# Kernel optimization log

Measured on AMD Instinct MI355X. Metric: run time of the kernel, lower is better.

Reference implementation:

```python
import jax, jax.numpy as jnp
import numpy as np

HIDDEN = 1024
HEADS = 16
HEAD_DIM = HIDDEN // HEADS
B, T = 4, 2048


def setup_inputs() -> dict:
    key = jax.random.key(0)
    k_x, k_w1, k_b1, k_w2, k_b2 = jax.random.split(key, 5)
    lim1 = 1.0 / np.sqrt(HIDDEN)
    x = jax.random.normal(k_x, (B, T, HIDDEN), dtype=jnp.float32)
    # causal lower-triangular mask, broadcastable to [B, H, T, T]
    mask = jnp.tril(jnp.ones((T, T), dtype=jnp.int32))[None, None, :, :]
    # qkv_proj: Linear(HIDDEN, 3*HIDDEN); torch Linear: y = x @ W.T + b
    W_qkv = jax.random.uniform(k_w1, (3 * HIDDEN, HIDDEN), minval=-lim1, maxval=lim1, dtype=jnp.float32)
    b_qkv = jax.random.uniform(k_b1, (3 * HIDDEN,), minval=-lim1, maxval=lim1, dtype=jnp.float32)
    W_out = jax.random.uniform(k_w2, (HIDDEN, HIDDEN), minval=-lim1, maxval=lim1, dtype=jnp.float32)
    b_out = jax.random.uniform(k_b2, (HIDDEN,), minval=-lim1, maxval=lim1, dtype=jnp.float32)
    return {"x": x, "mask": mask, "W_qkv": W_qkv, "b_qkv": b_qkv, "W_out": W_out, "b_out": b_out}


def reference(x, mask, W_qkv, b_qkv, W_out, b_out):
    Bx, Tx, C = x.shape
    qkv = x @ W_qkv.T + b_qkv                      # [B, T, 3C]
    qkv = qkv.reshape(Bx, Tx, 3, HEADS, HEAD_DIM)
    qkv = jnp.transpose(qkv, (2, 0, 3, 1, 4))      # [3, B, H, T, Dh]
    Q, K, V = qkv[0], qkv[1], qkv[2]
    scale = 1.0 / np.sqrt(HEAD_DIM)
    scores = jnp.einsum('bhqd,bhkd->bhqk', Q, K) * scale  # [B, H, T, T]
    scores = jnp.where(mask == 0, -jnp.inf, scores)
    probs = jax.nn.softmax(scores, axis=-1)
    ctx = jnp.einsum('bhqk,bhkd->bhqd', probs, V)  # [B, H, T, Dh]
    ctx = jnp.transpose(ctx, (0, 2, 1, 3)).reshape(Bx, Tx, C)
    return ctx @ W_out.T + b_out
```

## Files before the change

### kernel.cpp

```cpp
#include <hip/hip_runtime.h>
#include <cstdint>
#include <cstddef>

#define B_ 4
#define T_ 2048
#define C_ 1024
#define H_ 16
#define D_ 64

typedef __attribute__((ext_vector_type(8))) __bf16 bf16x8;
typedef __attribute__((ext_vector_type(4))) float floatx4;

#define QSCL (0.125f * 1.44269504088896f)
#define FMAX 24.0f

__device__ __forceinline__ unsigned short f2bf(float f) {
  union { float f; unsigned int u; } v; v.f = f;
  unsigned int r = v.u + 0x7fffu + ((v.u >> 16) & 1u);
  return (unsigned short)(r >> 16);
}
__device__ __forceinline__ ushort4 pk4(float a, float b, float c, float d) {
  ushort4 u; u.x = f2bf(a); u.y = f2bf(b); u.z = f2bf(c); u.w = f2bf(d);
  return u;
}
__device__ __forceinline__ bf16x8 cvt8(float4 a, float4 b) {
  bf16x8 r;
  r[0] = a.x; r[1] = a.y; r[2] = a.z; r[3] = a.w;
  r[4] = b.x; r[5] = b.y; r[6] = b.z; r[7] = b.w;
  return r;
}
__device__ __forceinline__ unsigned pkbf2(float a, float b) {
  union { __bf16 h[2]; unsigned u; } w;
  w.h[0] = (__bf16)a; w.h[1] = (__bf16)b;
  return w.u;
}

__device__ __forceinline__ void gl_lds16(const void* g, void* l) {
  __builtin_amdgcn_global_load_lds(
      (const __attribute__((address_space(1))) unsigned int*)g,
      (__attribute__((address_space(3))) unsigned int*)l, 16, 0, 0);
}

__global__ __launch_bounds__(256)
void conv_bf16(const float* __restrict__ src, unsigned short* __restrict__ dst,
               int n8) {
  for (int i = blockIdx.x * 256 + threadIdx.x; i < n8; i += gridDim.x * 256) {
    const float4* s = (const float4*)src + 2 * (size_t)i;
    float4 a = s[0], b = s[1];
    ((bf16x8*)dst)[i] = cvt8(a, b);
  }
}

__global__ __launch_bounds__(256)
void conv_tri(const float* __restrict__ s1, unsigned short* __restrict__ d1, int n1,
              const float* __restrict__ s2, unsigned short* __restrict__ d2, int n2,
              const float* __restrict__ s3, unsigned short* __restrict__ d3, int n3) {
  for (int i = blockIdx.x * 256 + threadIdx.x; i < n1 + n2 + n3; i += gridDim.x * 256) {
    const float4* sp; bf16x8* dp;
    if (i < n1)           { sp = (const float4*)s1 + 2 * (size_t)i;       dp = (bf16x8*)d1 + i; }
    else if (i < n1 + n2) { int j = i - n1;      sp = (const float4*)s2 + 2 * (size_t)j; dp = (bf16x8*)d2 + j; }
    else                  { int j = i - n1 - n2; sp = (const float4*)s3 + 2 * (size_t)j; dp = (bf16x8*)d3 + j; }
    float4 a = sp[0], b = sp[1];
    *dp = cvt8(a, b);
  }
}

template<int EPI, int GATHER, int WBF>
__global__ __launch_bounds__(256, 2)
void gemm_bt(const unsigned short* __restrict__ Abf,
             const void* __restrict__ Wraw,
             const float* __restrict__ bias,
             float* __restrict__ out,
             unsigned short* __restrict__ qws,
             unsigned short* __restrict__ kws,
             unsigned short* __restrict__ vtws)
{
  alignas(16) __shared__ unsigned short As[2][128 * 64];
  alignas(16) __shared__ unsigned short Bs[2][WBF ? 128 * 64 : 128 * 72];
  const int tid  = threadIdx.x;
  const int lane = tid & 63;
  const int wid  = tid >> 6;
  const int col  = lane & 15;
  const int quad = lane >> 4;
  const int wm = (wid >> 1) << 6;
  const int wn = (wid & 1) << 6;
  const int bm = blockIdx.y << 7;
  const int bn = blockIdx.x << 7;

  const float* Wf          = (const float*)Wraw;
  const unsigned short* Wb = (const unsigned short*)Wraw;

  const int r0 = tid >> 3;
  const int c0 = tid & 7;

  floatx4 acc[4][4];
#pragma unroll
  for (int i = 0; i < 4; ++i)
#pragma unroll
    for (int j = 0; j < 4; ++j)
      acc[i][j] = (floatx4){0.f, 0.f, 0.f, 0.f};

#define GSTAGE(k0_, nb_)                                                      \
  do {                                                                        \
    _Pragma("unroll") for (int s = 0; s < 4; ++s) {                           \
      const int row  = (s << 5) + r0;                             \
      const int colE = ((c0 ^ (row & 7)) << 3);             \
      const unsigned short* gsrc;                                             \
      if (GATHER) {                                                           \
        const int m = bm + row;                                               \
        const int b = m >> 11, t = m & 2047;                                  \
        const int hh = (k0_) >> 6;                        \
        gsrc = Abf + ((((size_t)(b * 16 + hh) << 11) + t) << 6) + colE;       \
      } else {                                                                \
        gsrc = Abf + (size_t)(bm + row) * 1024 + (k0_) + colE;                \
      }                                                                       \
      gl_lds16(gsrc, (char*)&As[nb_][0] + (s << 12) + (wid << 10));           \
      if (WBF) {                                                              \
        const unsigned short* ws2 = Wb + (size_t)(bn + row) * 1024 + (k0_) + colE; \
        gl_lds16(ws2, (char*)&Bs[nb_][0] + (s << 12) + (wid << 10));          \
      } else {                                                                \
        const int kc = c0 << 3;                                               \
        const float* wsrc = &Wf[(size_t)(bn + row) * 1024 + (k0_) + kc];      \
        float4 w0 = *(const float4*)wsrc;                                     \
        float4 w1 = *(const float4*)(wsrc + 4);                               \
        *(bf16x8*)&Bs[nb_][row * 72 + kc] = cvt8(w0, w1);                     \
      }                                                                       \
    }                                                                         \
  } while (0)

  GSTAGE(0, 0);
  __syncthreads();

  for (int kt = 0; kt < 16; ++kt) {
    const int buf = kt & 1;
    if (kt + 1 < 16) GSTAGE((kt + 1) << 6, buf ^ 1);

#pragma unroll
    for (int kk = 0; kk < 64; kk += 32) {
      bf16x8 af[4], bfr[4];
#pragma unroll
      for (int i = 0; i < 4; ++i) {
        const int r = wm + i * 16 + col;
        af[i] = *(const bf16x8*)&As[buf][(r << 6) + ((kk + quad * 8) ^ ((r & 7) << 3))];
      }
#pragma unroll
      for (int j = 0; j < 4; ++j) {
        const int r = wn + j * 16 + col;
        if (WBF)
          bfr[j] = *(const bf16x8*)&Bs[buf][(r << 6) + ((kk + quad * 8) ^ ((r & 7) << 3))];
        else
          bfr[j] = *(const bf16x8*)&Bs[buf][r * 72 + kk + quad * 8];
      }
#pragma unroll
      for (int i = 0; i < 4; ++i)
#pragma unroll
        for (int j = 0; j < 4; ++j)
          acc[i][j] = __builtin_amdgcn_mfma_f32_16x16x32_bf16(af[i], bfr[j], acc[i][j], 0, 0, 0);
    }

    __syncthreads();
  }
#undef GSTAGE

#pragma unroll
  for (int i = 0; i < 4; ++i) {
    const int row = bm + wm + i * 16 + quad * 4;
#pragma unroll
    for (int j = 0; j < 4; ++j) {
      const int n  = bn + wn + j * 16 + col;
      const float bv = bias[n];
      float v[4];
#pragma unroll
      for (int r = 0; r < 4; ++r) v[r] = acc[i][j][r] + bv;

      if (EPI == 1) {
#pragma unroll
        for (int r = 0; r < 4; ++r)
          out[(size_t)(row + r) * 1024 + n] = v[r];
      } else {
        const int s   = n >> 10;
        const int rem = n & 1023;
        const int h   = rem >> 6;
        const int d   = rem & 63;
        const int b   = row >> 11;
        const int t   = row & 2047;
        const size_t bh = (size_t)(b * H_ + h);
        if (s == 0) {
#pragma unroll
          for (int r = 0; r < 4; ++r)
            qws[(bh * T_ + t + r) * D_ + d] = f2bf(v[r] * QSCL);
        } else if (s == 1) {
#pragma unroll
          for (int r = 0; r < 4; ++r)
            kws[(bh * T_ + t + r) * D_ + d] = f2bf(v[r]);
        } else {
          *(ushort4*)&vtws[(bh * D_ + d) * T_ + t] = pk4(v[0], v[1], v[2], v[3]);
        }
      }
    }
  }
}

__global__ __launch_bounds__(256, 2)
void attn_causal(unsigned short* __restrict__ qws,
                 const unsigned short* __restrict__ kws,
                 const unsigned short* __restrict__ vtws)
{
  alignas(16) __shared__ unsigned short Ks[2][64 * 64];
  alignas(16) __shared__ unsigned short Vs[2][64 * 64];
  const int tid  = threadIdx.x;
  const int lane = tid & 63;
  const int wid  = tid >> 6;
  const int col  = lane & 15;
  const int quad = lane >> 4;

  const int bh   = blockIdx.x & 63;
  const int band = 15 - (blockIdx.x >> 6);

  const unsigned short* Kp  = kws + (size_t)bh * T_ * D_;
  const unsigned short* Vtp = vtws + (size_t)bh * D_ * T_;

  bf16x8 vones;
#pragma unroll
  for (int i = 0; i < 8; ++i) vones[i] = (__bf16)1.0f;

  const int srow8 = lane >> 3;
  const int swz   = ((lane & 7) ^ srow8) << 3;

#define STAGE(kt_, b_)                                                        \
  do {                                                                        \
    _Pragma("unroll") for (int c2 = 0; c2 < 2; ++c2) {                        \
      const int cb = wid + (c2 << 2);                   \
      gl_lds16(Kp + ((size_t)(((kt_) << 6) + (cb << 3) + srow8) << 6) + swz,  \
               (char*)&Ks[b_][0] + (cb << 10));                               \
      gl_lds16(Vtp + ((size_t)((cb << 3) + srow8) << 11) + ((kt_) << 6) + swz,\
               (char*)&Vs[b_][0] + (cb << 10));                               \
    }                                                                         \
  } while (0)

  const int nk = (band << 1) + 2;
  const int q0 = (band << 7) + (wid << 5);
  unsigned short* Qp = qws + ((size_t)bh * T_ + q0) * D_;

  bf16x8 bq[2][2];
#pragma unroll
  for (int h = 0; h < 2; ++h) {
    bq[h][0] = *(const bf16x8*)&Qp[(h * 16 + col) * D_ + quad * 8];
    bq[h][1] = *(const bf16x8*)&Qp[(h * 16 + col) * D_ + 32 + quad * 8];
  }

  floatx4 o[2][4], ol[2];
#pragma unroll
  for (int h = 0; h < 2; ++h) {
    ol[h] = (floatx4){0.f, 0.f, 0.f, 0.f};
#pragma unroll
    for (int j = 0; j < 4; ++j) o[h][j] = (floatx4){0.f, 0.f, 0.f, 0.f};
  }

  STAGE(0, 0);
  __syncthreads();

  for (int kt = 0; kt < nk; ++kt) {
    const int buf = kt & 1;
    if (kt + 1 < nk) STAGE(kt + 1, buf ^ 1);

    const unsigned short* Kb = &Ks[buf][0];
    bf16x8 kA[4], kB[4];
#pragma unroll
    for (int g = 0; g < 4; ++g) {
      const int r = g * 16 + col;
      kA[g] = *(const bf16x8*)&Kb[(r << 6) + ((quad ^ (col & 7)) << 3)];
      kB[g] = *(const bf16x8*)&Kb[(r << 6) + (((quad | 4) ^ (col & 7)) << 3)];
    }

    floatx4 s[2][4];
    __builtin_amdgcn_s_setprio(1);
#pragma unroll
    for (int h = 0; h < 2; ++h)
#pragma unroll
      for (int g = 0; g < 4; ++g) {
        s[h][g] = (floatx4){-FMAX, -FMAX, -FMAX, -FMAX};
        s[h][g] = __builtin_amdgcn_mfma_f32_16x16x32_bf16(kA[g], bq[h][0], s[h][g], 0, 0, 0);
        s[h][g] = __builtin_amdgcn_mfma_f32_16x16x32_bf16(kB[g], bq[h][1], s[h][g], 0, 0, 0);
      }
    __builtin_amdgcn_s_setprio(0);

    const unsigned short* Vb = &Vs[buf][0];
    bf16x8 vA[4], vB[4];
#pragma unroll
    for (int j = 0; j < 4; ++j) {
      const int r = j * 16 + col;
      vA[j] = *(const bf16x8*)&Vb[(r << 6) + ((quad ^ (col & 7)) << 3)];
      vB[j] = *(const bf16x8*)&Vb[(r << 6) + (((quad | 4) ^ (col & 7)) << 3)];
    }

    if (kt >= nk - 2) {
#pragma unroll
      for (int h = 0; h < 2; ++h) {
        const int lim = q0 - (kt << 6) + (h << 4) + col;
#pragma unroll
        for (int g = 0; g < 4; ++g)
#pragma unroll
          for (int r = 0; r < 4; ++r)
            if (g * 16 + quad * 4 + r > lim) s[h][g][r] = -1e30f;
      }
    }

#pragma unroll
    for (int h = 0; h < 2; ++h)
#pragma unroll
      for (int g = 0; g < 4; ++g)
#pragma unroll
        for (int r = 0; r < 4; ++r)
          s[h][g][r] = __builtin_amdgcn_exp2f(s[h][g][r]);

    __builtin_amdgcn_s_setprio(1);
#pragma unroll
    for (int h = 0; h < 2; ++h) {
      unsigned dw[4][2];
#pragma unroll
      for (int g = 0; g < 4; ++g) {
        dw[g][0] = pkbf2(s[h][g][0], s[h][g][1]);
        dw[g][1] = pkbf2(s[h][g][2], s[h][g][3]);
      }
      unsigned aw[4], bw[4];
      {
        auto t = __builtin_amdgcn_permlane32_swap(dw[0][0], dw[1][0], false, false);
        auto u = __builtin_amdgcn_permlane16_swap(t[0], t[1], false, false);
        aw[0] = u[0]; aw[2] = u[1];
      }
      {
        auto t = __builtin_amdgcn_permlane32_swap(dw[0][1], dw[1][1], false, false);
        auto u = __builtin_amdgcn_permlane16_swap(t[0], t[1], false, false);
        aw[1] = u[0]; aw[3] = u[1];
      }
      {
        auto t = __builtin_amdgcn_permlane32_swap(dw[2][0], dw[3][0], false, false);
        auto u = __builtin_amdgcn_permlane16_swap(t[0], t[1], false, false);
        bw[0] = u[0]; bw[2] = u[1];
      }
      {
        auto t = __builtin_amdgcn_permlane32_swap(dw[2][1], dw[3][1], false, false);
        auto u = __builtin_amdgcn_permlane16_swap(t[0], t[1], false, false);
        bw[1] = u[0]; bw[3] = u[1];
      }
      union { unsigned u[4]; bf16x8 v; } pa0, pa1;
#pragma unroll
      for (int w = 0; w < 4; ++w) { pa0.u[w] = aw[w]; pa1.u[w] = bw[w]; }

#pragma unroll
      for (int j = 0; j < 4; ++j) {
        o[h][j] = __builtin_amdgcn_mfma_f32_16x16x32_bf16(pa0.v, vA[j], o[h][j], 0, 0, 0);
        o[h][j] = __builtin_amdgcn_mfma_f32_16x16x32_bf16(pa1.v, vB[j], o[h][j], 0, 0, 0);
      }
      ol[h] = __builtin_amdgcn_mfma_f32_16x16x32_bf16(pa0.v, vones, ol[h], 0, 0, 0);
      ol[h] = __builtin_amdgcn_mfma_f32_16x16x32_bf16(pa1.v, vones, ol[h], 0, 0, 0);
    }
    __builtin_amdgcn_s_setprio(0);

    __syncthreads();
  }

#pragma unroll
  for (int h = 0; h < 2; ++h) {
    float lr[4];
#pragma unroll
    for (int r = 0; r < 4; ++r) lr[r] = 1.0f / ol[h][r];
#pragma unroll
    for (int j = 0; j < 4; ++j)
#pragma unroll
      for (int r = 0; r < 4; ++r)
        Qp[(size_t)(h * 16 + quad * 4 + r) * D_ + j * 16 + col] =
            f2bf(o[h][j][r] * lr[r]);
  }
#undef STAGE
}

extern "C" void kernel_launch(void* const* d_in, const int* in_sizes, int n_in,
                              void* d_out, int out_size, void* d_ws, size_t ws_size,
                              hipStream_t stream) {
  const float* x     = (const float*)d_in[0];
  const float* W_qkv = (const float*)d_in[2];
  const float* b_qkv = (const float*)d_in[3];
  const float* W_out = (const float*)d_in[4];
  const float* b_out = (const float*)d_in[5];
  float* out = (float*)d_out;

  const size_t per = (size_t)B_ * H_ * T_ * D_;
  unsigned short* qws  = (unsigned short*)d_ws;
  unsigned short* vtws = qws + per;
  unsigned short* kws  = (unsigned short*)d_out;
  unsigned short* xbf  = kws + per;

  const bool bigws  = ws_size >= (size_t)38 * 1024 * 1024;
  const bool hugews = ws_size >= (size_t)40 * 1024 * 1024;
  unsigned short* wqbf = vtws + per;
  unsigned short* wobf = wqbf + (size_t)3 * C_ * C_;

  if (hugews) {
    conv_tri<<<dim3(2048), 256, 0, stream>>>(
        x, xbf, (int)(per >> 3),
        W_qkv, wqbf, (3 * C_ * C_) >> 3,
        W_out, wobf, (C_ * C_) >> 3);
    gemm_bt<0, 0, 1><<<dim3(3072 / 128, 8192 / 128), 256, 0, stream>>>(
        xbf, (const void*)wqbf, b_qkv, nullptr, qws, kws, vtws);
  } else if (bigws) {
    conv_tri<<<dim3(2048), 256, 0, stream>>>(
        x, xbf, (int)(per >> 3),
        W_qkv, wqbf, (3 * C_ * C_) >> 3,
        nullptr, nullptr, 0);
    gemm_bt<0, 0, 1><<<dim3(3072 / 128, 8192 / 128), 256, 0, stream>>>(
        xbf, (const void*)wqbf, b_qkv, nullptr, qws, kws, vtws);
  } else {
    conv_bf16<<<dim3(2048), 256, 0, stream>>>(x, xbf, (int)(per >> 3));
    gemm_bt<0, 0, 0><<<dim3(3072 / 128, 8192 / 128), 256, 0, stream>>>(
        xbf, (const void*)W_qkv, b_qkv, nullptr, qws, kws, vtws);
  }

  attn_causal<<<dim3(16 * 64), 256, 0, stream>>>(qws, kws, vtws);

  if (hugews) {
    gemm_bt<1, 1, 1><<<dim3(1024 / 128, 8192 / 128), 256, 0, stream>>>(
        qws, (const void*)wobf, b_out, out, nullptr, nullptr, nullptr);
  } else {
    conv_bf16<<<dim3(512), 256, 0, stream>>>(W_out, vtws, (C_ * C_) >> 3);
    gemm_bt<1, 1, 1><<<dim3(1024 / 128, 8192 / 128), 256, 0, stream>>>(
        qws, (const void*)vtws, b_out, out, nullptr, nullptr, nullptr);
  }
}
```

Baseline: 247.3 us.

## Enlarge attention query tile to 256 rows per block with per-wave diagonal skip

Each attention block now covers 256 query rows instead of 128, with each wave handling 64 rows split into four 16-row groups processed in two pairs. K/V tiles staged in LDS are therefore reused by twice as many queries, which halves global K/V traffic. Waves skip key tiles past their own diagonal, and only the diagonal tile is masked. The cost is half as many blocks (512), more registers per wave, and load imbalance because waves within a block finish causal work at different tile counts while still waiting at the barriers.

After: 261.9 us. +5.9%, slower.

```diff
diff --git a/kernel.cpp b/kernel.cpp
--- a/kernel.cpp
+++ b/kernel.cpp
@@ -215,7 +215,7 @@
   const int quad = lane >> 4;
 
   const int bh   = blockIdx.x & 63;
-  const int band = 15 - (blockIdx.x >> 6);
+  const int band = 7 - (blockIdx.x >> 6);
 
   const unsigned short* Kp  = kws + (size_t)bh * T_ * D_;
   const unsigned short* Vtp = vtws + (size_t)bh * D_ * T_;
@@ -238,20 +238,21 @@
     }                                                                         \
   } while (0)
 
-  const int nk = (band << 1) + 2;
-  const int q0 = (band << 7) + (wid << 5);
+  const int nk    = (band + 1) << 2;
+  const int kdiag = (band << 2) + wid;
+  const int q0    = (band << 8) + (wid << 6);
   unsigned short* Qp = qws + ((size_t)bh * T_ + q0) * D_;
 
-  bf16x8 bq[2][2];
-#pragma unroll
-  for (int h = 0; h < 2; ++h) {
+  bf16x8 bq[4][2];
+#pragma unroll
+  for (int h = 0; h < 4; ++h) {
     bq[h][0] = *(const bf16x8*)&Qp[(h * 16 + col) * D_ + quad * 8];
     bq[h][1] = *(const bf16x8*)&Qp[(h * 16 + col) * D_ + 32 + quad * 8];
   }
 
-  floatx4 o[2][4], ol[2];
-#pragma unroll
-  for (int h = 0; h < 2; ++h) {
+  floatx4 o[4][4], ol[4];
+#pragma unroll
+  for (int h = 0; h < 4; ++h) {
     ol[h] = (floatx4){0.f, 0.f, 0.f, 0.f};
 #pragma unroll
     for (int j = 0; j < 4; ++j) o[h][j] = (floatx4){0.f, 0.f, 0.f, 0.f};
@@ -264,105 +265,112 @@
     const int buf = kt & 1;
     if (kt + 1 < nk) STAGE(kt + 1, buf ^ 1);
 
-    const unsigned short* Kb = &Ks[buf][0];
-    bf16x8 kA[4], kB[4];
-#pragma unroll
-    for (int g = 0; g < 4; ++g) {
-      const int r = g * 16 + col;
-      kA[g] = *(const bf16x8*)&Kb[(r << 6) + ((quad ^ (col & 7)) << 3)];
-      kB[g] = *(const bf16x8*)&Kb[(r << 6) + (((quad | 4) ^ (col & 7)) << 3)];
+    if (kt <= kdiag) {
+      const unsigned short* Kb = &Ks[buf][0];
+      bf16x8 kA[4], kB[4];
+#pragma unroll
+      for (int g = 0; g < 4; ++g) {
+        const int r = g * 16 + col;
+        kA[g] = *(const bf16x8*)&Kb[(r << 6) + ((quad ^ (col & 7)) << 3)];
+        kB[g] = *(const bf16x8*)&Kb[(r << 6) + (((quad | 4) ^ (col & 7)) << 3)];
+      }
+      const unsigned short* Vb = &Vs[buf][0];
+      bf16x8 vA[4], vB[4];
+#pragma unroll
+      for (int j = 0; j < 4; ++j) {
+        const int r = j * 16 + col;
+        vA[j] = *(const bf16x8*)&Vb[(r << 6) + ((quad ^ (col & 7)) << 3)];
+        vB[j] = *(const bf16x8*)&Vb[(r << 6) + (((quad | 4) ^ (col & 7)) << 3)];
+      }
+
+#pragma unroll
+      for (int hp = 0; hp < 2; ++hp) {
+        floatx4 s[2][4];
+        __builtin_amdgcn_s_setprio(1);
+#pragma unroll
+        for (int hh = 0; hh < 2; ++hh) {
+          const int h = hp * 2 + hh;
+#pragma unroll
+          for (int g = 0; g < 4; ++g) {
+            s[hh][g] = (floatx4){-FMAX, -FMAX, -FMAX, -FMAX};
+            s[hh][g] = __builtin_amdgcn_mfma_f32_16x16x32_bf16(kA[g], bq[h][0], s[hh][g], 0, 0, 0);
+            s[hh][g] = __builtin_amdgcn_mfma_f32_16x16x32_bf16(kB[g], bq[h][1], s[hh][g], 0, 0, 0);
+          }
+        }
+        __builtin_amdgcn_s_setprio(0);
+
+        if (kt == kdiag) {
+#pragma unroll
+          for (int hh = 0; hh < 2; ++hh) {
+            const int lim = ((hp * 2 + hh) << 4) + col;
+#pragma unroll
+            for (int g = 0; g < 4; ++g)
+#pragma unroll
+              for (int r = 0; r < 4; ++r)
+                if (g * 16 + quad * 4 + r > lim) s[hh][g][r] = -1e30f;
+          }
+        }
+
+#pragma unroll
+        for (int hh = 0; hh < 2; ++hh)
+#pragma unroll
+          for (int g = 0; g < 4; ++g)
+#pragma unroll
+            for (int r = 0; r < 4; ++r)
+              s[hh][g][r] = __builtin_amdgcn_exp2f(s[hh][g][r]);
+
+        __builtin_amdgcn_s_setprio(1);
+#pragma unroll
+        for (int hh = 0; hh < 2; ++hh) {
+          const int h = hp * 2 + hh;
+          unsigned dw[4][2];
+#pragma unroll
+          for (int g = 0; g < 4; ++g) {
+            dw[g][0] = pkbf2(s[hh][g][0], s[hh][g][1]);
+            dw[g][1] = pkbf2(s[hh][g][2], s[hh][g][3]);
+          }
+          unsigned aw[4], bw[4];
+          {
+            auto t = __builtin_amdgcn_permlane32_swap(dw[0][0], dw[1][0], false, false);
+            auto u = __builtin_amdgcn_permlane16_swap(t[0], t[1], false, false);
+            aw[0] = u[0]; aw[2] = u[1];
+          }
+          {
+            auto t = __builtin_amdgcn_permlane32_swap(dw[0][1], dw[1][1], false, false);
+            auto u = __builtin_amdgcn_permlane16_swap(t[0], t[1], false, false);
+            aw[1] = u[0]; aw[3] = u[1];
+          }
+          {
+            auto t = __builtin_amdgcn_permlane32_swap(dw[2][0], dw[3][0], false, false);
+            auto u = __builtin_amdgcn_permlane16_swap(t[0], t[1], false, false);
+            bw[0] = u[0]; bw[2] = u[1];
+          }
+          {
+            auto t = __builtin_amdgcn_permlane32_swap(dw[2][1], dw[3][1], false, false);
+            auto u = __builtin_amdgcn_permlane16_swap(t[0], t[1], false, false);
+            bw[1] = u[0]; bw[3] = u[1];
+          }
+          union { unsigned u[4]; bf16x8 v; } pa0, pa1;
+#pragma unroll
+          for (int w = 0; w < 4; ++w) { pa0.u[w] = aw[w]; pa1.u[w] = bw[w]; }
+
+#pragma unroll
+          for (int j = 0; j < 4; ++j) {
+            o[h][j] = __builtin_amdgcn_mfma_f32_16x16x32_bf16(pa0.v, vA[j], o[h][j], 0, 0, 0);
+            o[h][j] = __builtin_amdgcn_mfma_f32_16x16x32_bf16(pa1.v, vB[j], o[h][j], 0, 0, 0);
+          }
+          ol[h] = __builtin_amdgcn_mfma_f32_16x16x32_bf16(pa0.v, vones, ol[h], 0, 0, 0);
+          ol[h] = __builtin_amdgcn_mfma_f32_16x16x32_bf16(pa1.v, vones, ol[h], 0, 0, 0);
+        }
+        __builtin_amdgcn_s_setprio(0);
+      }
     }
 
-    floatx4 s[2][4];
-    __builtin_amdgcn_s_setprio(1);
-#pragma unroll
-    for (int h = 0; h < 2; ++h)
-#pragma unroll
-      for (int g = 0; g < 4; ++g) {
-        s[h][g] = (floatx4){-FMAX, -FMAX, -FMAX, -FMAX};
-        s[h][g] = __builtin_amdgcn_mfma_f32_16x16x32_bf16(kA[g], bq[h][0], s[h][g], 0, 0, 0);
-        s[h][g] = __builtin_amdgcn_mfma_f32_16x16x32_bf16(kB[g], bq[h][1], s[h][g], 0, 0, 0);
-      }
-    __builtin_amdgcn_s_setprio(0);
-
-    const unsigned short* Vb = &Vs[buf][0];
-    bf16x8 vA[4], vB[4];
-#pragma unroll
-    for (int j = 0; j < 4; ++j) {
-      const int r = j * 16 + col;
-      vA[j] = *(const bf16x8*)&Vb[(r << 6) + ((quad ^ (col & 7)) << 3)];
-      vB[j] = *(const bf16x8*)&Vb[(r << 6) + (((quad | 4) ^ (col & 7)) << 3)];
-    }
-
-    if (kt >= nk - 2) {
-#pragma unroll
-      for (int h = 0; h < 2; ++h) {
-        const int lim = q0 - (kt << 6) + (h << 4) + col;
-#pragma unroll
-        for (int g = 0; g < 4; ++g)
-#pragma unroll
-          for (int r = 0; r < 4; ++r)
-            if (g * 16 + quad * 4 + r > lim) s[h][g][r] = -1e30f;
-      }
-    }
-
-#pragma unroll
-    for (int h = 0; h < 2; ++h)
-#pragma unroll
-      for (int g = 0; g < 4; ++g)
-#pragma unroll
-        for (int r = 0; r < 4; ++r)
-          s[h][g][r] = __builtin_amdgcn_exp2f(s[h][g][r]);
-
-    __builtin_amdgcn_s_setprio(1);
-#pragma unroll
-    for (int h = 0; h < 2; ++h) {
-      unsigned dw[4][2];
-#pragma unroll
-      for (int g = 0; g < 4; ++g) {
-        dw[g][0] = pkbf2(s[h][g][0], s[h][g][1]);
-        dw[g][1] = pkbf2(s[h][g][2], s[h][g][3]);
-      }
-      unsigned aw[4], bw[4];
-      {
-        auto t = __builtin_amdgcn_permlane32_swap(dw[0][0], dw[1][0], false, false);
-        auto u = __builtin_amdgcn_permlane16_swap(t[0], t[1], false, false);
-        aw[0] = u[0]; aw[2] = u[1];
-      }
-      {
-        auto t = __builtin_amdgcn_permlane32_swap(dw[0][1], dw[1][1], false, false);
-        auto u = __builtin_amdgcn_permlane16_swap(t[0], t[1], false, false);
-        aw[1] = u[0]; aw[3] = u[1];
-      }
-      {
-        auto t = __builtin_amdgcn_permlane32_swap(dw[2][0], dw[3][0], false, false);
-        auto u = __builtin_amdgcn_permlane16_swap(t[0], t[1], false, false);
-        bw[0] = u[0]; bw[2] = u[1];
-      }
-      {
-        auto t = __builtin_amdgcn_permlane32_swap(dw[2][1], dw[3][1], false, false);
-        auto u = __builtin_amdgcn_permlane16_swap(t[0], t[1], false, false);
-        bw[1] = u[0]; bw[3] = u[1];
-      }
-      union { unsigned u[4]; bf16x8 v; } pa0, pa1;
-#pragma unroll
-      for (int w = 0; w < 4; ++w) { pa0.u[w] = aw[w]; pa1.u[w] = bw[w]; }
-
-#pragma unroll
-      for (int j = 0; j < 4; ++j) {
-        o[h][j] = __builtin_amdgcn_mfma_f32_16x16x32_bf16(pa0.v, vA[j], o[h][j], 0, 0, 0);
-        o[h][j] = __builtin_amdgcn_mfma_f32_16x16x32_bf16(pa1.v, vB[j], o[h][j], 0, 0, 0);
-      }
-      ol[h] = __builtin_amdgcn_mfma_f32_16x16x32_bf16(pa0.v, vones, ol[h], 0, 0, 0);
-      ol[h] = __builtin_amdgcn_mfma_f32_16x16x32_bf16(pa1.v, vones, ol[h], 0, 0, 0);
-    }
-    __builtin_amdgcn_s_setprio(0);
-
     __syncthreads();
   }
 
 #pragma unroll
-  for (int h = 0; h < 2; ++h) {
+  for (int h = 0; h < 4; ++h) {
     float lr[4];
 #pragma unroll
     for (int r = 0; r < 4; ++r) lr[r] = 1.0f / ol[h][r];
@@ -417,7 +425,7 @@
         xbf, (const void*)W_qkv, b_qkv, nullptr, qws, kws, vtws);
   }
 
-  attn_causal<<<dim3(16 * 64), 256, 0, stream>>>(qws, kws, vtws);
+  attn_causal<<<dim3(8 * 64), 256, 0, stream>>>(qws, kws, vtws);
 
   if (hugews) {
     gemm_bt<1, 1, 1><<<dim3(1024 / 128, 8192 / 128), 256, 0, stream>>>(
```
